# Kernel tuning notes

Measured on AMD Instinct MI355X. Metric: run time of the kernel, lower is better.

## Reference

```python
import jax, jax.numpy as jnp
import numpy as np

D_MODEL = 512
D_STATE = 64
D_INNER = 2 * D_MODEL   # standard Mamba expand=2
D_CONV = 4
DT_RANK = D_MODEL // 16  # 32
LN_EPS = 1e-5


def setup_inputs() -> dict:
    key = jax.random.key(0)
    ks = jax.random.split(key, 12)
    B, L = 2, 1024
    s = 0.02
    return {
        "frames": jax.random.normal(ks[0], (B, L, D_MODEL), jnp.float32),
        "gamma": jnp.ones((D_MODEL,), jnp.float32),
        "beta": jnp.zeros((D_MODEL,), jnp.float32),
        "W_in": jax.random.normal(ks[1], (D_MODEL, 2 * D_INNER), jnp.float32) * s,
        "conv_w": jax.random.normal(ks[2], (D_INNER, D_CONV), jnp.float32) * s,
        "conv_b": jnp.zeros((D_INNER,), jnp.float32),
        "W_x": jax.random.normal(ks[3], (D_INNER, DT_RANK + 2 * D_STATE), jnp.float32) * s,
        "W_dt": jax.random.normal(ks[4], (DT_RANK, D_INNER), jnp.float32) * s,
        "b_dt": jax.random.uniform(ks[5], (D_INNER,), jnp.float32, -4.0, -2.0),
        "A_log": jnp.log(jnp.broadcast_to(jnp.arange(1, D_STATE + 1, dtype=jnp.float32), (D_INNER, D_STATE))),
        "D": jnp.ones((D_INNER,), jnp.float32),
        "W_out": jax.random.normal(ks[6], (D_INNER, D_MODEL), jnp.float32) * s,
    }


def reference(frames, gamma, beta, W_in, conv_w, conv_b, W_x, W_dt, b_dt, A_log, D, W_out):
    B, L, _ = frames.shape
    d_inner = W_in.shape[1] // 2
    d_state = A_log.shape[1]
    dt_rank = W_dt.shape[0]
    d_conv = conv_w.shape[1]

    # LayerNorm
    mu = frames.mean(-1, keepdims=True)
    var = ((frames - mu) ** 2).mean(-1, keepdims=True)
    xn = (frames - mu) * jax.lax.rsqrt(var + LN_EPS) * gamma + beta

    # in_proj -> x, z
    x, z = jnp.split(xn @ W_in, 2, axis=-1)  # each (B, L, d_inner)

    # causal depthwise conv1d along time
    xc = jnp.pad(x.transpose(0, 2, 1), ((0, 0), (0, 0), (d_conv - 1, 0)))  # (B, d_inner, L+pad)
    xconv = jax.lax.conv_general_dilated(
        xc, conv_w[:, None, :], (1,), "VALID", feature_group_count=d_inner)  # (B, d_inner, L)
    x = jax.nn.silu(xconv.transpose(0, 2, 1) + conv_b)  # (B, L, d_inner)

    # input-dependent dt, B, C
    xdb = x @ W_x
    dt, Bm, Cm = jnp.split(xdb, [dt_rank, dt_rank + d_state], axis=-1)
    delta = jax.nn.softplus(dt @ W_dt + b_dt)  # (B, L, d_inner)
    A = -jnp.exp(A_log)                        # (d_inner, d_state)

    # selective scan over time
    def step(h, inp):
        d_t, B_t, C_t, x_t = inp  # (B,d_inner) (B,d_state) (B,d_state) (B,d_inner)
        dA = jnp.exp(d_t[..., None] * A)                       # (B,d_inner,d_state)
        h = h * dA + (d_t * x_t)[..., None] * B_t[:, None, :]  # (B,d_inner,d_state)
        y = jnp.einsum("bds,bs->bd", h, C_t)
        return h, y

    h0 = jnp.zeros((B, d_inner, d_state), frames.dtype)
    xs = (delta.transpose(1, 0, 2), Bm.transpose(1, 0, 2),
          Cm.transpose(1, 0, 2), x.transpose(1, 0, 2))
    _, ys = jax.lax.scan(step, h0, xs)  # (L, B, d_inner)

    y = ys.transpose(1, 0, 2) + x * D
    y = y * jax.nn.silu(z)
    return y @ W_out + frames  # residual connection
```

## Files before the change

kernel.cpp:

```cpp
#include <hip/hip_runtime.h>
#include <hip/hip_bf16.h>
#include <math.h>

constexpr int Bn     = 2;
constexpr int Lseq   = 1024;
constexpr int DM     = 512;
constexpr int DI     = 1024;
constexpr int DS     = 64;
constexpr int RNK    = 32;
constexpr int NROWS  = Bn * Lseq;
constexpr int XDBW   = RNK + 2 * DS;
constexpr int CH     = 64;
constexpr int NC     = Lseq / CH;

constexpr float LOG2E = 1.44269504088896340736f;

typedef __attribute__((ext_vector_type(4))) float floatx4;
typedef __attribute__((ext_vector_type(8))) short shortx8;

__device__ __forceinline__ float silu_f(float v) {
    return v / (1.f + __expf(-v));
}

__device__ __forceinline__ float rdl(float v, int l) {
    return __int_as_float(__builtin_amdgcn_readlane(__float_as_int(v), l));
}

__device__ __forceinline__ float bf2f(unsigned short u) {
    return __uint_as_float((unsigned)u << 16);
}

__device__ __forceinline__ float exp2_fast(float x) {
#if __has_builtin(__builtin_amdgcn_exp2f)
    return __builtin_amdgcn_exp2f(x);
#else
    return exp2f(x);
#endif
}

__global__ void prep_kernel(const float* __restrict__ x, const float* __restrict__ g,
                            const float* __restrict__ be,
                            const float* __restrict__ Wi, const float* __restrict__ Wo,
                            const float* __restrict__ Wx,
                            __hip_bfloat16* __restrict__ xn,
                            __hip_bfloat16* __restrict__ Ti, __hip_bfloat16* __restrict__ To,
                            __hip_bfloat16* __restrict__ Tx) {
    __shared__ float tile[64][65];
    __shared__ float red[8];
    int bid = blockIdx.x;
    int tid = threadIdx.x;
    if (bid < NROWS) {
        int row = bid;
        const float* xr = x + (size_t)row * DM;
        float v0 = xr[tid], v1 = xr[tid + 256];
        float s = v0 + v1, sq = v0 * v0 + v1 * v1;
        #pragma unroll
        for (int o = 1; o < 64; o <<= 1) {
            s  += __shfl_xor(s, o);
            sq += __shfl_xor(sq, o);
        }
        int w = tid >> 6;
        if ((tid & 63) == 0) { red[w] = s; red[4 + w] = sq; }
        __syncthreads();
        float ts = red[0] + red[1] + red[2] + red[3];
        float tq = red[4] + red[5] + red[6] + red[7];
        float mu  = ts * (1.f / DM);
        float var = tq * (1.f / DM) - mu * mu;
        float inv = rsqrtf(var + 1e-5f);
        __hip_bfloat16* o0 = xn + (size_t)row * DM;
        o0[tid]       = __float2bfloat16((v0 - mu) * inv * g[tid]       + be[tid]);
        o0[tid + 256] = __float2bfloat16((v1 - mu) * inv * g[tid + 256] + be[tid + 256]);
        return;
    }
    int b2 = bid - NROWS;
    const float* in; __hip_bfloat16* out; int R, Cc, bx, by;
    if (b2 < 256)      { in = Wi; out = Ti; R = DM; Cc = 2 * DI; bx = b2 & 31; by = b2 >> 5; }
    else if (b2 < 384) { int b3 = b2 - 256; in = Wo; out = To; R = DI; Cc = DM;   bx = b3 & 7; by = b3 >> 3; }
    else               { int b3 = b2 - 384; in = Wx; out = Tx; R = DI; Cc = XDBW; bx = b3 % 3; by = b3 / 3; }
    int r0 = by * 64, c0 = bx * 64;
    #pragma unroll
    for (int i = tid; i < 4096; i += 256) {
        int r = i >> 6, c = i & 63;
        tile[r][c] = (r0 + r < R && c0 + c < Cc) ? in[(size_t)(r0 + r) * Cc + c0 + c] : 0.f;
    }
    __syncthreads();
    #pragma unroll
    for (int i = tid; i < 4096; i += 256) {
        int c = i >> 6, r = i & 63;
        if (r0 + r < R && c0 + c < Cc)
            out[(size_t)(c0 + c) * R + r0 + r] = __float2bfloat16(tile[r][c]);
    }
}

__global__ __launch_bounds__(512) void gemm_inproj(const __hip_bfloat16* __restrict__ A,
                                                   const __hip_bfloat16* __restrict__ Bt,
                                                   __hip_bfloat16* __restrict__ xh,
                                                   __hip_bfloat16* __restrict__ zh,
                                                   int M, int N, int K) {
    __shared__ __hip_bfloat16 As[128 * 64];
    __shared__ __hip_bfloat16 Bs[128 * 64];
    const int tid  = threadIdx.x;
    const int wave = tid >> 6, lane = tid & 63;
    const int m0 = blockIdx.y * 128, n0 = blockIdx.x * 128;
    const int wm = (wave >> 2) * 64, wn = (wave & 3) * 32;

    floatx4 acc[4][2] = {};

    const int arow16 = lane & 15;
    const int kgrp   = lane >> 4;

    for (int k0 = 0; k0 < K; k0 += 64) {
        #pragma unroll
        for (int p = 0; p < 2; ++p) {
            int j = tid + p * 512;
            int h = j >> 9, rs = j & 511;
            int row = rs >> 2, seg = rs & 3;
            const __hip_bfloat16* gA = A  + (size_t)(m0 + row) * K + k0 + h * 32 + seg * 8;
            const __hip_bfloat16* gB = Bt + (size_t)(n0 + row) * K + k0 + h * 32 + seg * 8;
            __hip_bfloat16* lA = As + (size_t)(wave * 64 + p * 512) * 8;
            __hip_bfloat16* lB = Bs + (size_t)(wave * 64 + p * 512) * 8;
            __builtin_amdgcn_global_load_lds(
                (const __attribute__((address_space(1))) void*)gA,
                (__attribute__((address_space(3))) void*)lA, 16, 0, 0);
            __builtin_amdgcn_global_load_lds(
                (const __attribute__((address_space(1))) void*)gB,
                (__attribute__((address_space(3))) void*)lB, 16, 0, 0);
        }
        __syncthreads();

        const shortx8* Asv = (const shortx8*)As;
        const shortx8* Bsv = (const shortx8*)Bs;
        #pragma unroll
        for (int h = 0; h < 2; ++h) {
            shortx8 a[4], b[2];
            #pragma unroll
            for (int i = 0; i < 4; ++i)
                a[i] = Asv[h * 512 + (wm + i * 16 + arow16) * 4 + kgrp];
            #pragma unroll
            for (int j = 0; j < 2; ++j)
                b[j] = Bsv[h * 512 + (wn + j * 16 + arow16) * 4 + kgrp];
            #pragma unroll
            for (int i = 0; i < 4; ++i)
                #pragma unroll
                for (int j = 0; j < 2; ++j)
                    acc[i][j] = __builtin_amdgcn_mfma_f32_16x16x32_bf16(a[i], b[j], acc[i][j], 0, 0, 0);
        }
        __syncthreads();
    }

    const int drow = (lane >> 4) * 4;
    const int dcol = lane & 15;
    const bool isz = (n0 >= DI);
    __hip_bfloat16* dst = isz ? zh : xh;
    const int coloff = isz ? DI : 0;
    #pragma unroll
    for (int i = 0; i < 4; ++i)
        #pragma unroll
        for (int j = 0; j < 2; ++j) {
            int rowb = m0 + wm + i * 16 + drow;
            int col  = n0 + wn + j * 16 + dcol - coloff;
            #pragma unroll
            for (int r = 0; r < 4; ++r)
                dst[(size_t)(rowb + r) * DI + col] = __float2bfloat16(acc[i][j][r]);
        }
}

template<bool RES>
__global__ __launch_bounds__(512) void gemm64_sk(const __hip_bfloat16* __restrict__ A,
                                                 const __hip_bfloat16* __restrict__ Bt,
                                                 const float* __restrict__ Res,
                                                 float* __restrict__ C,
                                                 int M, int N, int K) {
    __shared__ __hip_bfloat16 As[2][64 * 64];
    __shared__ __hip_bfloat16 Bs[2][64 * 64];
    __shared__ float red[256 * 17];
    const int tid  = threadIdx.x;
    const int wave = tid >> 6, lane = tid & 63;
    const int g = wave >> 2, w2 = wave & 3;
    const int m0 = blockIdx.y * 64, n0 = blockIdx.x * 64;
    const int wm = (w2 >> 1) * 32, wn = (w2 & 1) * 32;

    floatx4 acc[2][2] = {};

    const int arow16 = lane & 15;
    const int kgrp   = lane >> 4;
    const int kbeg   = g * (K / 2);

    for (int kk = 0; kk < K / 2; kk += 64) {
        int k0 = kbeg + kk;
        #pragma unroll
        for (int p = 0; p < 2; ++p) {
            int j = (w2 * 64 + lane) + p * 256;
            int h = j >> 8, rs = j & 255;
            int row = rs >> 2, seg = rs & 3;
            int brow = n0 + row; if (brow >= N) brow = N - 1;
            const __hip_bfloat16* gA = A  + (size_t)(m0 + row) * K + k0 + h * 32 + seg * 8;
            const __hip_bfloat16* gB = Bt + (size_t)brow * K + k0 + h * 32 + seg * 8;
            __hip_bfloat16* lA = As[g] + (size_t)(w2 * 64 + p * 256) * 8;
            __hip_bfloat16* lB = Bs[g] + (size_t)(w2 * 64 + p * 256) * 8;
            __builtin_amdgcn_global_load_lds(
                (const __attribute__((address_space(1))) void*)gA,
                (__attribute__((address_space(3))) void*)lA, 16, 0, 0);
            __builtin_amdgcn_global_load_lds(
                (const __attribute__((address_space(1))) void*)gB,
                (__attribute__((address_space(3))) void*)lB, 16, 0, 0);
        }
        __syncthreads();

        const shortx8* Asv = (const shortx8*)As[g];
        const shortx8* Bsv = (const shortx8*)Bs[g];
        #pragma unroll
        for (int h = 0; h < 2; ++h) {
            shortx8 a[2], b[2];
            #pragma unroll
            for (int i = 0; i < 2; ++i)
                a[i] = Asv[h * 256 + (wm + i * 16 + arow16) * 4 + kgrp];
            #pragma unroll
            for (int j = 0; j < 2; ++j)
                b[j] = Bsv[h * 256 + (wn + j * 16 + arow16) * 4 + kgrp];
            #pragma unroll
            for (int i = 0; i < 2; ++i)
                #pragma unroll
                for (int j = 0; j < 2; ++j)
                    acc[i][j] = __builtin_amdgcn_mfma_f32_16x16x32_bf16(a[i], b[j], acc[i][j], 0, 0, 0);
        }
        __syncthreads();
    }

    int rbase = (w2 * 64 + lane) * 17;
    if (g == 1) {
        #pragma unroll
        for (int i = 0; i < 2; ++i)
            #pragma unroll
            for (int j = 0; j < 2; ++j)
                *(float4*)&red[rbase + (i * 2 + j) * 4] =
                    make_float4(acc[i][j][0], acc[i][j][1], acc[i][j][2], acc[i][j][3]);
    }
    __syncthreads();
    if (g == 0) {
        const int drow = (lane >> 4) * 4;
        const int dcol = lane & 15;
        #pragma unroll
        for (int i = 0; i < 2; ++i)
            #pragma unroll
            for (int j = 0; j < 2; ++j) {
                float4 part = *(const float4*)&red[rbase + (i * 2 + j) * 4];
                int rowb = m0 + wm + i * 16 + drow;
                int col  = n0 + wn + j * 16 + dcol;
                if (col < N) {
                    #pragma unroll
                    for (int r = 0; r < 4; ++r) {
                        size_t idx = (size_t)(rowb + r) * N + col;
                        float v = acc[i][j][r] + (&part.x)[r];
                        if (RES) v += Res[idx];
                        C[idx] = v;
                    }
                }
            }
    }
}

__global__ __launch_bounds__(256) void conv_tile(const __hip_bfloat16* __restrict__ xh,
                                                 const __hip_bfloat16* __restrict__ zh,
                                                 const float* __restrict__ cw,
                                                 const float* __restrict__ cb,
                                                 __hip_bfloat16* __restrict__ xcv_bf,
                                                 __hip_bfloat16* __restrict__ xcvT,
                                                 __hip_bfloat16* __restrict__ zgT) {
    __shared__ float xt[67][68];
    __shared__ float tb[64][65];
    __shared__ float tb2[64][65];
    int t0 = blockIdx.x * 64, d0 = blockIdx.y * 64, b = blockIdx.z;
    int tid = threadIdx.x;
    size_t rowbase = (size_t)b * Lseq;

    for (int i = tid; i < 67 * 16; i += 256) {
        int r = i >> 4, j = i & 15;
        int t = t0 - 3 + r;
        float4 v4 = make_float4(0.f, 0.f, 0.f, 0.f);
        if (t >= 0) {
            ushort4 u = *(const ushort4*)&xh[(rowbase + t) * DI + d0 + j * 4];
            v4 = make_float4(bf2f(u.x), bf2f(u.y), bf2f(u.z), bf2f(u.w));
        }
        *(float4*)&xt[r][j * 4] = v4;
    }
    for (int i = tid; i < 64 * 16; i += 256) {
        int r = i >> 4, j = i & 15;
        ushort4 u = *(const ushort4*)&zh[(rowbase + t0 + r) * DI + d0 + j * 4];
        tb2[r][j * 4 + 0] = silu_f(bf2f(u.x));
        tb2[r][j * 4 + 1] = silu_f(bf2f(u.y));
        tb2[r][j * 4 + 2] = silu_f(bf2f(u.z));
        tb2[r][j * 4 + 3] = silu_f(bf2f(u.w));
    }
    __syncthreads();

    {
        int d = tid & 63, tg = tid >> 6;
        float4 cwv = *(const float4*)&cw[(d0 + d) * 4];
        float cbv = cb[d0 + d];
        #pragma unroll
        for (int i = 0; i < 16; ++i) {
            int t = tg * 16 + i;
            float acc = cbv;
            #pragma unroll
            for (int k = 0; k < 4; ++k) acc += xt[t + k][d] * (&cwv.x)[k];
            float v = silu_f(acc);
            tb[t][d] = v;
            xcv_bf[(rowbase + t0 + t) * DI + d0 + d] = __float2bfloat16(v);
        }
    }
    __syncthreads();

    {
        int t2 = tid & 63, dg2 = tid >> 6;
        #pragma unroll
        for (int i = 0; i < 16; ++i) {
            int d = dg2 * 16 + i;
            size_t orow = ((size_t)(b * DI + d0 + d)) * Lseq + t0 + t2;
            xcvT[orow] = __float2bfloat16(tb[t2][d]);
            zgT[orow]  = __float2bfloat16(tb2[t2][d]);
        }
    }
}

__global__ void delta_kernel(const float* __restrict__ xdb, const float* __restrict__ Wdt,
                             const float* __restrict__ bdt, float* __restrict__ delta) {
    int row = blockIdx.y;
    int d = blockIdx.x * 256 + threadIdx.x;
    __shared__ float dtv[RNK];
    if (threadIdx.x < RNK) dtv[threadIdx.x] = xdb[(size_t)row * XDBW + threadIdx.x];
    __syncthreads();
    float acc = bdt[d];
    #pragma unroll
    for (int r = 0; r < RNK; ++r) acc += dtv[r] * Wdt[(size_t)r * DI + d];
    float sp = (acc > 20.f) ? acc : log1pf(__expf(acc));
    delta[(size_t)row * DI + d] = sp;
}

__global__ __launch_bounds__(512) void scan_chunk1(
        const float* __restrict__ delta, const __hip_bfloat16* __restrict__ xcvT,
        const float* __restrict__ xdb, const float* __restrict__ A_log,
        float* __restrict__ hend, float* __restrict__ dsum) {
    __shared__ float Bsh[64][68];
    __shared__ float dsh[16][65];

    int blk = blockIdx.x;
    int dg  = blk & 63;
    int bc  = blk >> 6;
    int c = bc & (NC - 1), b = bc >> 4;
    int tid = threadIdx.x, w = tid >> 6, lane = tid & 63;
    int dbase = dg * 16;
    int r0 = b * Lseq + c * CH;

    #pragma unroll
    for (int k = 0; k < 2; ++k) {
        int idx = tid + k * 512;
        int row = idx >> 4, j4 = idx & 15;
        float4 v = *(const float4*)&xdb[(size_t)(r0 + row) * XDBW + RNK + j4 * 4];
        *(float4*)&Bsh[row][j4 * 4] = v;
    }
    #pragma unroll
    for (int k = 0; k < 2; ++k) {
        int i = tid + k * 512;
        int dd = i & 15, t = i >> 4;
        dsh[dd][t] = delta[(size_t)(r0 + t) * DI + dbase + dd];
    }
    __syncthreads();

    int d0 = dbase + w, d1 = dbase + 8 + w;
    float a0 = -__expf(A_log[d0 * DS + lane]) * LOG2E;
    float a1 = -__expf(A_log[d1 * DS + lane]) * LOG2E;
    float vd0 = dsh[w][lane],     vd1 = dsh[8 + w][lane];
    float xv0 = bf2f(((const unsigned short*)xcvT)[
        ((size_t)(b * DI + d0)) * Lseq + c * CH + lane]);
    float xv1 = bf2f(((const unsigned short*)xcvT)[
        ((size_t)(b * DI + d1)) * Lseq + c * CH + lane]);
    float vpx0 = vd0 * xv0, vpx1 = vd1 * xv1;
    float h0 = 0.f, h1 = 0.f;
    #pragma unroll 16
    for (int t = 0; t < CH; ++t) {
        float Bt = Bsh[t][lane];
        h0 = h0 * exp2_fast(rdl(vd0, t) * a0) + rdl(vpx0, t) * Bt;
        h1 = h1 * exp2_fast(rdl(vd1, t) * a1) + rdl(vpx1, t) * Bt;
    }
    float S0 = vd0, S1 = vd1;
    #pragma unroll
    for (int o = 1; o < 64; o <<= 1) {
        S0 += __shfl_xor(S0, o);
        S1 += __shfl_xor(S1, o);
    }
    size_t cb = (size_t)bc * DI;
    hend[(cb + d0) * 64 + lane] = h0;
    hend[(cb + d1) * 64 + lane] = h1;
    if (lane == 0) {
        dsum[cb + d0] = S0;
        dsum[cb + d1] = S1;
    }
}

__global__ __launch_bounds__(512) void scan_chunk2(
        const float* __restrict__ delta, const __hip_bfloat16* __restrict__ xcvT,
        const float* __restrict__ xdb, const __hip_bfloat16* __restrict__ zgT,
        const float* __restrict__ A_log, const float* __restrict__ Dp,
        const float* __restrict__ hend, const float* __restrict__ dsum,
        __hip_bfloat16* __restrict__ y_row) {
    __shared__ float2 BC[64][66];
    __shared__ float dsh[8][64];
    __shared__ float P[8][8 * 65];

    int blk = blockIdx.x;
    int dg  = blk & (DI / 8 - 1);
    int bc  = blk >> 7;
    int c = bc & (NC - 1), b = bc >> 4;
    int tid = threadIdx.x, w = tid >> 6, lane = tid & 63;
    int d = dg * 8 + w;
    int r0 = b * Lseq + c * CH;

    #pragma unroll
    for (int k = 0; k < 2; ++k) {
        int i = tid + k * 512;
        int t = i >> 4, sg = i & 15;
        const float* rowp = &xdb[(size_t)(r0 + t) * XDBW + RNK];
        float4 bv = *(const float4*)&rowp[sg * 4];
        float4 cv = *(const float4*)&rowp[DS + sg * 4];
        *(float4*)&BC[t][sg * 4]     = make_float4(bv.x, cv.x, bv.y, cv.y);
        *(float4*)&BC[t][sg * 4 + 2] = make_float4(bv.z, cv.z, bv.w, cv.w);
    }
    {
        int t = tid >> 3, ww = tid & 7;
        dsh[ww][t] = delta[(size_t)(r0 + t) * DI + dg * 8 + ww];
    }
    __syncthreads();

    float a2 = -__expf(A_log[d * DS + lane]) * LOG2E;
    float Dv = Dp[d];
    size_t trow = ((size_t)(b * DI + d)) * Lseq + c * CH + lane;
    float xv = bf2f(((const unsigned short*)xcvT)[trow]);
    float zv = bf2f(((const unsigned short*)zgT)[trow]);
    float vd  = dsh[w][lane];
    float vpx = vd * xv;

    float h = 0.f;
    for (int j = 0; j < c; ++j) {
        size_t cbj = (size_t)(b * NC + j) * DI + d;
        float he = hend[cbj * 64 + lane];
        float S  = dsum[cbj];
        h = he + exp2_fast(a2 * S) * h;
    }

    float* Pw = P[w];
    float yreg = 0.f;
    const int tr = lane & 7, q = lane >> 3;

    #pragma unroll
    for (int t8 = 0; t8 < 8; ++t8) {
        #pragma unroll
        for (int tt = 0; tt < 8; ++tt) {
            int t = t8 * 8 + tt;
            float2 bcv = BC[t][lane];
            float dt_ = rdl(vd, t);
            float px  = rdl(vpx, t);
            h = h * exp2_fast(dt_ * a2) + px * bcv.x;
            Pw[tt * 65 + lane] = h * bcv.y;
        }
        float sacc = 0.f;
        #pragma unroll
        for (int j = 0; j < 8; ++j) sacc += Pw[tr * 65 + q * 8 + j];
        sacc += __shfl_xor(sacc, 8);
        sacc += __shfl_xor(sacc, 16);
        sacc += __shfl_xor(sacc, 32);
        if (q == t8) yreg = sacc;
    }

    float yv = (yreg + xv * Dv) * zv;

    __syncthreads();
    float* T = (float*)P;
    T[lane * 9 + w] = yv;
    __syncthreads();
    {
        int t = tid >> 3, dd = tid & 7;
        float v = T[t * 9 + dd];
        y_row[(size_t)(r0 + t) * DI + dg * 8 + dd] = __float2bfloat16(v);
    }
}

extern "C" void kernel_launch(void* const* d_in, const int* in_sizes, int n_in,
                              void* d_out, int out_size, void* d_ws, size_t ws_size,
                              hipStream_t stream) {
    const float* frames = (const float*)d_in[0];
    const float* gamma  = (const float*)d_in[1];
    const float* beta   = (const float*)d_in[2];
    const float* W_in   = (const float*)d_in[3];
    const float* conv_w = (const float*)d_in[4];
    const float* conv_b = (const float*)d_in[5];
    const float* W_x    = (const float*)d_in[6];
    const float* W_dt   = (const float*)d_in[7];
    const float* b_dt   = (const float*)d_in[8];
    const float* A_log  = (const float*)d_in[9];
    const float* Dp     = (const float*)d_in[10];
    const float* W_out  = (const float*)d_in[11];
    float* out = (float*)d_out;

    char* ws = (char*)d_ws;
    __hip_bfloat16* xn_bf  = (__hip_bfloat16*)ws; ws += (size_t)NROWS * DM * 2;
    __hip_bfloat16* Wt_in  = (__hip_bfloat16*)ws; ws += (size_t)(2 * DI) * DM * 2;
    __hip_bfloat16* Wt_out = (__hip_bfloat16*)ws; ws += (size_t)DM * DI * 2;
    __hip_bfloat16* Wt_x   = (__hip_bfloat16*)ws; ws += (size_t)XDBW * DI * 2;
    __hip_bfloat16* y_row  = (__hip_bfloat16*)ws; ws += (size_t)NROWS * DI * 2;
    __hip_bfloat16* xcv_bf = (__hip_bfloat16*)ws; ws += (size_t)NROWS * DI * 2;
    __hip_bfloat16* xh     = (__hip_bfloat16*)ws; ws += (size_t)NROWS * DI * 2;
    __hip_bfloat16* zh     = (__hip_bfloat16*)ws; ws += (size_t)NROWS * DI * 2;
    __hip_bfloat16* xcvT   = (__hip_bfloat16*)ws; ws += (size_t)NROWS * DI * 2;
    __hip_bfloat16* zgT    = (__hip_bfloat16*)ws; ws += (size_t)NROWS * DI * 2;
    float* xdb    = (float*)ws;  ws += (size_t)NROWS * XDBW * 4;
    float* delta  = (float*)ws;  ws += (size_t)NROWS * DI * 4;
    float* hend   = (float*)ws;  ws += (size_t)Bn * NC * DI * 64 * 4;
    float* dsum   = (float*)ws;  ws += (size_t)Bn * NC * DI * 4;

    prep_kernel<<<NROWS + 432, 256, 0, stream>>>(frames, gamma, beta, W_in, W_out, W_x,
                                                 xn_bf, Wt_in, Wt_out, Wt_x);

    gemm_inproj<<<dim3(2 * DI / 128, NROWS / 128), 512, 0, stream>>>(
        xn_bf, Wt_in, xh, zh, NROWS, 2 * DI, DM);

    conv_tile<<<dim3(Lseq / 64, DI / 64, Bn), 256, 0, stream>>>(
        xh, zh, conv_w, conv_b, xcv_bf, xcvT, zgT);

    gemm64_sk<false><<<dim3((XDBW + 63) / 64, NROWS / 64), 512, 0, stream>>>(
        xcv_bf, Wt_x, nullptr, xdb, NROWS, XDBW, DI);

    delta_kernel<<<dim3(DI / 256, NROWS), 256, 0, stream>>>(xdb, W_dt, b_dt, delta);

    scan_chunk1<<<Bn * NC * (DI / 16), 512, 0, stream>>>(delta, xcvT, xdb, A_log, hend, dsum);
    scan_chunk2<<<Bn * NC * (DI / 8), 512, 0, stream>>>(delta, xcvT, xdb, zgT, A_log, Dp,
                                                        hend, dsum, y_row);

    gemm64_sk<true><<<dim3(DM / 64, NROWS / 64), 512, 0, stream>>>(
        y_row, Wt_out, frames, out, NROWS, DM, DI);
}
```

Before: 230.4 us.

## Replace two-pass chunked scan with single sequential scan per channel group

Replaces the two-pass chunked selective scan (per-chunk end states plus a carry-in pass that loops over all prior chunks) with one kernel where each block walks all 16 chunks of a sequence in order. The next chunk's B, C, delta, x and z are prefetched into registers and double-buffered in shared memory. This removes the hend/dsum traffic, the extra launch and the redundant carry recomputation, at the cost of far fewer blocks (256 instead of 4096) and a serial chain of 1024 steps per block. The delta kernel also now handles 8 rows per block so each W_dt load is reused across rows.

```diff
diff --git a/kernel.cpp b/kernel.cpp
--- a/kernel.cpp
+++ b/kernel.cpp
@@ -12,6 +12,7 @@
 constexpr int XDBW   = RNK + 2 * DS;
 constexpr int CH     = 64;
 constexpr int NC     = Lseq / CH;
+constexpr int DROWS  = 8;
 
 constexpr float LOG2E = 1.44269504088896340736f;
 
@@ -323,165 +324,164 @@
     }
 }
 
-__global__ void delta_kernel(const float* __restrict__ xdb, const float* __restrict__ Wdt,
-                             const float* __restrict__ bdt, float* __restrict__ delta) {
-    int row = blockIdx.y;
+__global__ __launch_bounds__(256) void delta_kernel(const float* __restrict__ xdb,
+                                                    const float* __restrict__ Wdt,
+                                                    const float* __restrict__ bdt,
+                                                    float* __restrict__ delta) {
+    int r0 = blockIdx.y * DROWS;
     int d = blockIdx.x * 256 + threadIdx.x;
-    __shared__ float dtv[RNK];
-    if (threadIdx.x < RNK) dtv[threadIdx.x] = xdb[(size_t)row * XDBW + threadIdx.x];
+    __shared__ float dtv[RNK][DROWS];
+    if (threadIdx.x < DROWS * RNK) {
+        int k = threadIdx.x >> 5, r = threadIdx.x & 31;
+        dtv[r][k] = xdb[(size_t)(r0 + k) * XDBW + r];
+    }
     __syncthreads();
-    float acc = bdt[d];
+    float bb = bdt[d];
+    float acc[DROWS];
     #pragma unroll
-    for (int r = 0; r < RNK; ++r) acc += dtv[r] * Wdt[(size_t)r * DI + d];
-    float sp = (acc > 20.f) ? acc : log1pf(__expf(acc));
-    delta[(size_t)row * DI + d] = sp;
-}
-
-__global__ __launch_bounds__(512) void scan_chunk1(
-        const float* __restrict__ delta, const __hip_bfloat16* __restrict__ xcvT,
-        const float* __restrict__ xdb, const float* __restrict__ A_log,
-        float* __restrict__ hend, float* __restrict__ dsum) {
-    __shared__ float Bsh[64][68];
-    __shared__ float dsh[16][65];
-
-    int blk = blockIdx.x;
-    int dg  = blk & 63;
-    int bc  = blk >> 6;
-    int c = bc & (NC - 1), b = bc >> 4;
-    int tid = threadIdx.x, w = tid >> 6, lane = tid & 63;
-    int dbase = dg * 16;
-    int r0 = b * Lseq + c * CH;
-
+    for (int k = 0; k < DROWS; ++k) acc[k] = bb;
     #pragma unroll
-    for (int k = 0; k < 2; ++k) {
-        int idx = tid + k * 512;
-        int row = idx >> 4, j4 = idx & 15;
-        float4 v = *(const float4*)&xdb[(size_t)(r0 + row) * XDBW + RNK + j4 * 4];
-        *(float4*)&Bsh[row][j4 * 4] = v;
+    for (int r = 0; r < RNK; ++r) {
+        float wv = Wdt[(size_t)r * DI + d];
+        float4 lo = *(const float4*)&dtv[r][0];
+        float4 hi = *(const float4*)&dtv[r][4];
+        acc[0] += lo.x * wv; acc[1] += lo.y * wv;
+        acc[2] += lo.z * wv; acc[3] += lo.w * wv;
+        acc[4] += hi.x * wv; acc[5] += hi.y * wv;
+        acc[6] += hi.z * wv; acc[7] += hi.w * wv;
     }
     #pragma unroll
-    for (int k = 0; k < 2; ++k) {
-        int i = tid + k * 512;
-        int dd = i & 15, t = i >> 4;
-        dsh[dd][t] = delta[(size_t)(r0 + t) * DI + dbase + dd];
-    }
-    __syncthreads();
-
-    int d0 = dbase + w, d1 = dbase + 8 + w;
-    float a0 = -__expf(A_log[d0 * DS + lane]) * LOG2E;
-    float a1 = -__expf(A_log[d1 * DS + lane]) * LOG2E;
-    float vd0 = dsh[w][lane],     vd1 = dsh[8 + w][lane];
-    float xv0 = bf2f(((const unsigned short*)xcvT)[
-        ((size_t)(b * DI + d0)) * Lseq + c * CH + lane]);
-    float xv1 = bf2f(((const unsigned short*)xcvT)[
-        ((size_t)(b * DI + d1)) * Lseq + c * CH + lane]);
-    float vpx0 = vd0 * xv0, vpx1 = vd1 * xv1;
-    float h0 = 0.f, h1 = 0.f;
-    #pragma unroll 16
-    for (int t = 0; t < CH; ++t) {
-        float Bt = Bsh[t][lane];
-        h0 = h0 * exp2_fast(rdl(vd0, t) * a0) + rdl(vpx0, t) * Bt;
-        h1 = h1 * exp2_fast(rdl(vd1, t) * a1) + rdl(vpx1, t) * Bt;
-    }
-    float S0 = vd0, S1 = vd1;
-    #pragma unroll
-    for (int o = 1; o < 64; o <<= 1) {
-        S0 += __shfl_xor(S0, o);
-        S1 += __shfl_xor(S1, o);
-    }
-    size_t cb = (size_t)bc * DI;
-    hend[(cb + d0) * 64 + lane] = h0;
-    hend[(cb + d1) * 64 + lane] = h1;
-    if (lane == 0) {
-        dsum[cb + d0] = S0;
-        dsum[cb + d1] = S1;
-    }
-}
-
-__global__ __launch_bounds__(512) void scan_chunk2(
+    for (int k = 0; k < DROWS; ++k) {
+        float a = acc[k];
+        float sp = (a > 20.f) ? a : log1pf(__expf(a));
+        delta[(size_t)(r0 + k) * DI + d] = sp;
+    }
+}
+
+__global__ __launch_bounds__(512) void scan_full(
         const float* __restrict__ delta, const __hip_bfloat16* __restrict__ xcvT,
         const float* __restrict__ xdb, const __hip_bfloat16* __restrict__ zgT,
         const float* __restrict__ A_log, const float* __restrict__ Dp,
-        const float* __restrict__ hend, const float* __restrict__ dsum,
         __hip_bfloat16* __restrict__ y_row) {
-    __shared__ float2 BC[64][66];
-    __shared__ float dsh[8][64];
+    __shared__ float Bsh[2][64][65];
+    __shared__ float Csh[2][64][65];
+    __shared__ float dsh[2][64][9];
     __shared__ float P[8][8 * 65];
+    __shared__ float T[64 * 9];
 
     int blk = blockIdx.x;
-    int dg  = blk & (DI / 8 - 1);
-    int bc  = blk >> 7;
-    int c = bc & (NC - 1), b = bc >> 4;
+    int dg  = blk & 127;
+    int b   = blk >> 7;
     int tid = threadIdx.x, w = tid >> 6, lane = tid & 63;
     int d = dg * 8 + w;
-    int r0 = b * Lseq + c * CH;
-
-    #pragma unroll
-    for (int k = 0; k < 2; ++k) {
-        int i = tid + k * 512;
-        int t = i >> 4, sg = i & 15;
-        const float* rowp = &xdb[(size_t)(r0 + t) * XDBW + RNK];
-        float4 bv = *(const float4*)&rowp[sg * 4];
-        float4 cv = *(const float4*)&rowp[DS + sg * 4];
-        *(float4*)&BC[t][sg * 4]     = make_float4(bv.x, cv.x, bv.y, cv.y);
-        *(float4*)&BC[t][sg * 4 + 2] = make_float4(bv.z, cv.z, bv.w, cv.w);
-    }
-    {
-        int t = tid >> 3, ww = tid & 7;
-        dsh[ww][t] = delta[(size_t)(r0 + t) * DI + dg * 8 + ww];
-    }
-    __syncthreads();
 
     float a2 = -__expf(A_log[d * DS + lane]) * LOG2E;
     float Dv = Dp[d];
-    size_t trow = ((size_t)(b * DI + d)) * Lseq + c * CH + lane;
-    float xv = bf2f(((const unsigned short*)xcvT)[trow]);
-    float zv = bf2f(((const unsigned short*)zgT)[trow]);
-    float vd  = dsh[w][lane];
-    float vpx = vd * xv;
+
+    const int st_t = tid >> 3, st_d = tid & 7;
+
+    {
+        int r0 = b * Lseq;
+        #pragma unroll
+        for (int k = 0; k < 2; ++k) {
+            int i = tid + k * 512;
+            int t = i >> 4, sg = i & 15;
+            const float* rowp = &xdb[(size_t)(r0 + t) * XDBW + RNK];
+            *(float4*)&Bsh[0][t][sg * 4] = *(const float4*)&rowp[sg * 4];
+            *(float4*)&Csh[0][t][sg * 4] = *(const float4*)&rowp[DS + sg * 4];
+        }
+        dsh[0][st_t][st_d] = delta[(size_t)(r0 + st_t) * DI + dg * 8 + st_d];
+    }
+    __syncthreads();
+
+    const unsigned short* xT = (const unsigned short*)xcvT;
+    const unsigned short* zT = (const unsigned short*)zgT;
+    const size_t chbase = (size_t)(b * DI + d) * Lseq;
+
+    float xv = bf2f(xT[chbase + lane]);
+    float zv = bf2f(zT[chbase + lane]);
 
     float h = 0.f;
-    for (int j = 0; j < c; ++j) {
-        size_t cbj = (size_t)(b * NC + j) * DI + d;
-        float he = hend[cbj * 64 + lane];
-        float S  = dsum[cbj];
-        h = he + exp2_fast(a2 * S) * h;
-    }
-
     float* Pw = P[w];
-    float yreg = 0.f;
     const int tr = lane & 7, q = lane >> 3;
-
-    #pragma unroll
-    for (int t8 = 0; t8 < 8; ++t8) {
-        #pragma unroll
-        for (int tt = 0; tt < 8; ++tt) {
-            int t = t8 * 8 + tt;
-            float2 bcv = BC[t][lane];
-            float dt_ = rdl(vd, t);
-            float px  = rdl(vpx, t);
-            h = h * exp2_fast(dt_ * a2) + px * bcv.x;
-            Pw[tt * 65 + lane] = h * bcv.y;
-        }
-        float sacc = 0.f;
-        #pragma unroll
-        for (int j = 0; j < 8; ++j) sacc += Pw[tr * 65 + q * 8 + j];
-        sacc += __shfl_xor(sacc, 8);
-        sacc += __shfl_xor(sacc, 16);
-        sacc += __shfl_xor(sacc, 32);
-        if (q == t8) yreg = sacc;
-    }
-
-    float yv = (yreg + xv * Dv) * zv;
-
-    __syncthreads();
-    float* T = (float*)P;
-    T[lane * 9 + w] = yv;
-    __syncthreads();
-    {
-        int t = tid >> 3, dd = tid & 7;
-        float v = T[t * 9 + dd];
-        y_row[(size_t)(r0 + t) * DI + dg * 8 + dd] = __float2bfloat16(v);
+    const int rdbase = tr * 65 + q * 8;
+
+    for (int c = 0; c < NC; ++c) {
+        int cur = c & 1;
+
+        float4 pb0, pc0, pb1, pc1;
+        float pd = 0.f, nxv = 0.f, nzv = 0.f;
+        if (c + 1 < NC) {
+            int r1 = b * Lseq + (c + 1) * CH;
+            {
+                int t = tid >> 4, sg = tid & 15;
+                const float* rowp = &xdb[(size_t)(r1 + t) * XDBW + RNK];
+                pb0 = *(const float4*)&rowp[sg * 4];
+                pc0 = *(const float4*)&rowp[DS + sg * 4];
+            }
+            {
+                int i = tid + 512;
+                int t = i >> 4, sg = i & 15;
+                const float* rowp = &xdb[(size_t)(r1 + t) * XDBW + RNK];
+                pb1 = *(const float4*)&rowp[sg * 4];
+                pc1 = *(const float4*)&rowp[DS + sg * 4];
+            }
+            pd  = delta[(size_t)(r1 + st_t) * DI + dg * 8 + st_d];
+            nxv = bf2f(xT[chbase + (c + 1) * CH + lane]);
+            nzv = bf2f(zT[chbase + (c + 1) * CH + lane]);
+        }
+
+        int r0 = b * Lseq + c * CH;
+        float vd  = dsh[cur][lane][w];
+        float vpx = vd * xv;
+        float y = 0.f;
+
+        #pragma unroll
+        for (int t8 = 0; t8 < 8; ++t8) {
+            #pragma unroll
+            for (int tt = 0; tt < 8; ++tt) {
+                int t = t8 * 8 + tt;
+                float Bt = Bsh[cur][t][lane];
+                float Ct = Csh[cur][t][lane];
+                h = h * exp2_fast(rdl(vd, t) * a2) + rdl(vpx, t) * Bt;
+                Pw[tt * 65 + lane] = h * Ct;
+            }
+            float sacc = 0.f;
+            #pragma unroll
+            for (int j = 0; j < 8; ++j) sacc += Pw[rdbase + j];
+            sacc += __shfl_xor(sacc, 8);
+            sacc += __shfl_xor(sacc, 16);
+            sacc += __shfl_xor(sacc, 32);
+            if (q == t8) y = sacc;
+        }
+
+        float yv = (y + xv * Dv) * zv;
+
+        __syncthreads();
+        T[lane * 9 + w] = yv;
+        if (c + 1 < NC) {
+            int nxt = cur ^ 1;
+            {
+                int t = tid >> 4, sg = tid & 15;
+                *(float4*)&Bsh[nxt][t][sg * 4] = pb0;
+                *(float4*)&Csh[nxt][t][sg * 4] = pc0;
+            }
+            {
+                int i = tid + 512;
+                int t = i >> 4, sg = i & 15;
+                *(float4*)&Bsh[nxt][t][sg * 4] = pb1;
+                *(float4*)&Csh[nxt][t][sg * 4] = pc1;
+            }
+            dsh[nxt][st_t][st_d] = pd;
+        }
+        __syncthreads();
+
+        {
+            float v = T[st_t * 9 + st_d];
+            y_row[(size_t)(r0 + st_t) * DI + dg * 8 + st_d] = __float2bfloat16(v);
+        }
+
+        xv = nxv; zv = nzv;
     }
 }
 
@@ -515,8 +515,6 @@
     __hip_bfloat16* zgT    = (__hip_bfloat16*)ws; ws += (size_t)NROWS * DI * 2;
     float* xdb    = (float*)ws;  ws += (size_t)NROWS * XDBW * 4;
     float* delta  = (float*)ws;  ws += (size_t)NROWS * DI * 4;
-    float* hend   = (float*)ws;  ws += (size_t)Bn * NC * DI * 64 * 4;
-    float* dsum   = (float*)ws;  ws += (size_t)Bn * NC * DI * 4;
 
     prep_kernel<<<NROWS + 432, 256, 0, stream>>>(frames, gamma, beta, W_in, W_out, W_x,
                                                  xn_bf, Wt_in, Wt_out, Wt_x);
@@ -530,11 +528,9 @@
     gemm64_sk<false><<<dim3((XDBW + 63) / 64, NROWS / 64), 512, 0, stream>>>(
         xcv_bf, Wt_x, nullptr, xdb, NROWS, XDBW, DI);
 
-    delta_kernel<<<dim3(DI / 256, NROWS), 256, 0, stream>>>(xdb, W_dt, b_dt, delta);
-
-    scan_chunk1<<<Bn * NC * (DI / 16), 512, 0, stream>>>(delta, xcvT, xdb, A_log, hend, dsum);
-    scan_chunk2<<<Bn * NC * (DI / 8), 512, 0, stream>>>(delta, xcvT, xdb, zgT, A_log, Dp,
-                                                        hend, dsum, y_row);
+    delta_kernel<<<dim3(DI / 256, NROWS / DROWS), 256, 0, stream>>>(xdb, W_dt, b_dt, delta);
+
+    scan_full<<<Bn * (DI / 8), 512, 0, stream>>>(delta, xcvT, xdb, zgT, A_log, Dp, y_row);
 
     gemm64_sk<true><<<dim3(DM / 64, NROWS / 64), 512, 0, stream>>>(
         y_row, Wt_out, frames, out, NROWS, DM, DI);
```

New measurement: 220.7 us. -4.2%, faster.
